# Kernel optimization log

Hardware: AMD Instinct MI355X
Metric: run time of the kernel (lower is better)

## Reference

```python
import jax, jax.numpy as jnp
import numpy as np

N_LVL = [131072, 32768, 8192, 2048, 512, 256]  # active voxels per pyramid level
B = 8          # point clouds in batch
K = 27         # 3x3x3 kernel offsets
SLOPE = 0.01   # LeakyReLU default negative slope
EPS = 1e-5     # BatchNorm eps


def _bn(x, g, b):
    # MinkowskiBatchNorm, training-mode forward: stats over all points
    m = x.mean(0)
    v = x.var(0)
    return (x - m) * jax.lax.rsqrt(v + EPS) * g + b


def _lrelu(x):
    return jnp.where(x >= 0, x, SLOPE * x)


def _lin_block(x, w, g, b):
    # MinkowskiLinear(bias=False) + BN + LeakyReLU (also models 1x1 conv)
    return _lrelu(_bn(x @ w, g, b))


def _conv_block(x, nbr, w, g, b):
    # sparse conv as gather-GEMM: [N,K,Cin] x [K,Cin,Cout] -> [N,Cout]
    y = jnp.einsum('nkc,kco->no', x[nbr], w)
    return _lrelu(_bn(y, g, b))


def _maxpool(x, pmap):
    # stride-2 kernel-3 sparse max pool via precomputed pooling map
    return x[pmap].max(axis=1)


def setup_inputs() -> dict:
    key = jax.random.key(0)
    ks = iter(jax.random.split(key, 80))

    def nrm(shape, scale):
        return jax.random.normal(next(ks), shape, dtype=jnp.float32) * jnp.float32(scale)

    inp = {}
    inp['x'] = nrm((N_LVL[0], 3), 1.0)
    inp['w_mlp1'] = nrm((3, 16), 1.0 / np.sqrt(3.0))
    inp['g_mlp1'] = jnp.ones(16, jnp.float32)
    inp['b_mlp1'] = jnp.zeros(16, jnp.float32)
    conv_dims = [(16, 32), (32, 48), (48, 96), (96, 128), (128, 256), (256, 512)]
    down_dims = [(48, 32), (80, 48), (144, 96), (224, 128), (384, 256)]
    for i, (ci, co) in enumerate(conv_dims):
        inp[f'w_c{i+1}'] = nrm((K, ci, co), np.sqrt(2.0 / (K * co)))  # kaiming fan_out
        inp[f'g_c{i+1}'] = jnp.ones(co, jnp.float32)
        inp[f'b_c{i+1}'] = jnp.zeros(co, jnp.float32)
    for i, (ci, co) in enumerate(down_dims):
        inp[f'w_d{i+1}'] = nrm((ci, co), np.sqrt(2.0 / co))
        inp[f'g_d{i+1}'] = jnp.ones(co, jnp.float32)
        inp[f'b_d{i+1}'] = jnp.zeros(co, jnp.float32)
    inp['w_f1'] = nrm((1024, 512), 1.0 / 32.0)
    inp['g_f1'] = jnp.ones(512, jnp.float32)
    inp['b_f1'] = jnp.zeros(512, jnp.float32)
    inp['w_f2'] = nrm((512, 256), 1.0 / np.sqrt(512.0))
    inp['g_f2'] = jnp.ones(256, jnp.float32)
    inp['b_f2'] = jnp.zeros(256, jnp.float32)
    inp['w_f3'] = nrm((256, 20), 1.0 / 16.0)
    inp['bias_f3'] = jnp.zeros(20, jnp.float32)
    for i in range(6):
        inp[f'nbr{i}'] = jax.random.randint(next(ks), (N_LVL[i], K), 0, N_LVL[i], dtype=jnp.int32)
    for i in range(1, 6):
        inp[f'pool{i}'] = jax.random.randint(next(ks), (N_LVL[i], K), 0, N_LVL[i - 1], dtype=jnp.int32)
    inp['batch5'] = jnp.repeat(jnp.arange(B, dtype=jnp.int32), N_LVL[5] // B)
    return inp


def reference(x, w_mlp1, g_mlp1, b_mlp1,
              w_c1, g_c1, b_c1, w_c2, g_c2, b_c2, w_c3, g_c3, b_c3,
              w_c4, g_c4, b_c4, w_c5, g_c5, b_c5, w_c6, g_c6, b_c6,
              w_d1, g_d1, b_d1, w_d2, g_d2, b_d2, w_d3, g_d3, b_d3,
              w_d4, g_d4, b_d4, w_d5, g_d5, b_d5,
              w_f1, g_f1, b_f1, w_f2, g_f2, b_f2, w_f3, bias_f3,
              nbr0, nbr1, nbr2, nbr3, nbr4, nbr5,
              pool1, pool2, pool3, pool4, pool5, batch5):
    convs = [(w_c1, g_c1, b_c1), (w_c2, g_c2, b_c2), (w_c3, g_c3, b_c3),
             (w_c4, g_c4, b_c4), (w_c5, g_c5, b_c5)]
    downs = [(w_d1, g_d1, b_d1), (w_d2, g_d2, b_d2), (w_d3, g_d3, b_d3),
             (w_d4, g_d4, b_d4), (w_d5, g_d5, b_d5)]
    nbrs = [nbr0, nbr1, nbr2, nbr3, nbr4]
    pools = [pool1, pool2, pool3, pool4, pool5]

    y = _lin_block(x, w_mlp1, g_mlp1, b_mlp1)  # mlp1, level 0
    for i in range(5):  # fixed 5 conv/cat/down/pool stages (structural loop)
        out = _conv_block(y, nbrs[i], *convs[i])
        y = _lin_block(jnp.concatenate([y, out], axis=1), *downs[i])  # cat + down (1x1)
        y = _maxpool(y, pools[i])
    y = _conv_block(y, nbr5, w_c6, g_c6, b_c6)  # conv6 at level 5: [N5, 512]

    xmax = jax.ops.segment_max(y, batch5, num_segments=B)
    cnt = jax.ops.segment_sum(jnp.ones((y.shape[0], 1), y.dtype), batch5, num_segments=B)
    xavg = jax.ops.segment_sum(y, batch5, num_segments=B) / cnt
    z = jnp.concatenate([xmax, xavg], axis=1)  # [B, 1024]

    z = _lin_block(z, w_f1, g_f1, b_f1)  # dropout = identity (eval)
    z = _lin_block(z, w_f2, g_f2, b_f2)
    return z @ w_f3 + bias_f3  # [B, 20] logits
```

## Files before the change

kernel.cpp:

```cpp
#include <hip/hip_runtime.h>
#include <math.h>


#define SLOPE 0.01f
#define BN_EPS 1e-5f

__device__ __forceinline__ void fma4(float s, const float4& w, float4& a) {
    a.x = fmaf(s, w.x, a.x);
    a.y = fmaf(s, w.y, a.y);
    a.z = fmaf(s, w.z, a.z);
    a.w = fmaf(s, w.w, a.w);
}

__global__ void zero_kernel(float* __restrict__ p, int n) {
    int i = blockIdx.x * blockDim.x + threadIdx.x;
    if (i < n) p[i] = 0.f;
}

__global__ void lin_kernel(const float* __restrict__ in, const float* __restrict__ w,
                           float* __restrict__ out, int total, int Cin, int Cout) {
    int stride = gridDim.x * blockDim.x;
    for (int i = blockIdx.x * blockDim.x + threadIdx.x; i < total; i += stride) {
        int n = i / Cout;
        int co = i - n * Cout;
        const float* row = in + n * Cin;
        float acc = 0.f;
        for (int ci = 0; ci < Cin; ci++)
            acc = fmaf(row[ci], w[ci * Cout + co], acc);
        out[i] = acc;
    }
}

__global__ void stats_kernel(const float* __restrict__ x, int total, int C,
                             float* __restrict__ sums) {
    __shared__ float ls[1024];
    int tid = threadIdx.x;
    for (int i = tid; i < 2 * C; i += blockDim.x) ls[i] = 0.f;
    __syncthreads();
    int stride = gridDim.x * blockDim.x;
    int i = blockIdx.x * blockDim.x + tid;
    int c = i % C;
    float s = 0.f, q = 0.f;
    for (; i < total; i += stride) {
        float v = x[i];
        s += v;
        q = fmaf(v, v, q);
    }
    atomicAdd(&ls[c], s);
    atomicAdd(&ls[C + c], q);
    __syncthreads();
    for (int j = tid; j < 2 * C; j += blockDim.x)
        atomicAdd(&sums[j], ls[j]);
}

__global__ void bn_apply_kernel(float* __restrict__ x, int total, int C,
                                const float* __restrict__ sums,
                                const float* __restrict__ g, const float* __restrict__ b,
                                float inv_n) {
    int stride = gridDim.x * blockDim.x;
    for (int i = blockIdx.x * blockDim.x + threadIdx.x; i < total; i += stride) {
        int c = i % C;
        float mean = sums[c] * inv_n;
        float var = fmaf(-mean, mean, sums[C + c] * inv_n);
        var = fmaxf(var, 0.f);
        float scale = g[c] * rsqrtf(var + BN_EPS);
        float v = fmaf(x[i] - mean, scale, b[c]);
        x[i] = v >= 0.f ? v : SLOPE * v;
    }
}

__global__ void maxpool_kernel(const float* __restrict__ in, const int* __restrict__ pmap,
                               float* __restrict__ out, int total, int C) {
    int stride = gridDim.x * blockDim.x;
    for (int i = blockIdx.x * blockDim.x + threadIdx.x; i < total; i += stride) {
        int n = i / C;
        int c = i - n * C;
        const int* pm = pmap + n * 27;
        float m = -INFINITY;
        #pragma unroll
        for (int k = 0; k < 27; k++)
            m = fmaxf(m, in[pm[k] * C + c]);
        out[i] = m;
    }
}

template <int C1, int C2, int COUT>
__global__ void down2_kernel(const float* __restrict__ in1, const float* __restrict__ in2,
                             const float* __restrict__ w, float* __restrict__ out, int Nrows) {
    constexpr int CQT = COUT / 4;
    int i = blockIdx.x * blockDim.x + threadIdx.x;
    if (i >= Nrows * CQT) return;
    int n = i / CQT;
    int coq = i - n * CQT;
    const float4* w4 = reinterpret_cast<const float4*>(w);
    float4 acc = make_float4(0.f, 0.f, 0.f, 0.f);
    const float4* r1 = reinterpret_cast<const float4*>(in1 + n * C1);
    #pragma unroll
    for (int j = 0; j < C1 / 4; j++) {
        float4 a = r1[j];
        fma4(a.x, w4[(4 * j + 0) * CQT + coq], acc);
        fma4(a.y, w4[(4 * j + 1) * CQT + coq], acc);
        fma4(a.z, w4[(4 * j + 2) * CQT + coq], acc);
        fma4(a.w, w4[(4 * j + 3) * CQT + coq], acc);
    }
    const float4* r2 = reinterpret_cast<const float4*>(in2 + n * C2);
    #pragma unroll
    for (int j = 0; j < C2 / 4; j++) {
        float4 a = r2[j];
        int ci = C1 + 4 * j;
        fma4(a.x, w4[(ci + 0) * CQT + coq], acc);
        fma4(a.y, w4[(ci + 1) * CQT + coq], acc);
        fma4(a.z, w4[(ci + 2) * CQT + coq], acc);
        fma4(a.w, w4[(ci + 3) * CQT + coq], acc);
    }
    reinterpret_cast<float4*>(out)[i] = acc;
}

template <int CIN, int COUT, int TM, int CO_TILE, int KT, int NTHR, bool ATOMIC>
__global__ __launch_bounds__(NTHR) void conv2_kernel(
    const float* __restrict__ y, const int* __restrict__ nbr,
    const float* __restrict__ w, float* __restrict__ out) {
    constexpr int CQ = CO_TILE / 4;
    constexpr int MGRP = NTHR / CQ;
    constexpr int RT = TM / MGRP;
    constexpr int LROW = CIN + 4;
    __shared__ __align__(16) float a[TM * LROW];

    const int m0 = blockIdx.x * TM;
    const int cobase = blockIdx.y * CO_TILE;
    const int k0 = blockIdx.z * KT;
    const int tid = threadIdx.x;
    const int coq = tid % CQ;
    const int mg = tid / CQ;

    float4 acc[RT];
    #pragma unroll
    for (int r = 0; r < RT; r++) acc[r] = make_float4(0.f, 0.f, 0.f, 0.f);

    for (int k = k0; k < k0 + KT; k++) {
        __syncthreads();
        for (int idx = tid; idx < TM * (CIN / 4); idx += NTHR) {
            int m = idx / (CIN / 4);
            int c4 = idx - m * (CIN / 4);
            int row = nbr[(m0 + m) * 27 + k];
            float4 v = *reinterpret_cast<const float4*>(y + row * CIN + c4 * 4);
            *reinterpret_cast<float4*>(&a[m * LROW + c4 * 4]) = v;
        }
        __syncthreads();
        const float* wk = w + k * CIN * COUT + cobase + coq * 4;
        #pragma unroll
        for (int ci = 0; ci < CIN; ci += 4) {
            float4 w0 = *reinterpret_cast<const float4*>(wk + (ci + 0) * COUT);
            float4 w1 = *reinterpret_cast<const float4*>(wk + (ci + 1) * COUT);
            float4 w2 = *reinterpret_cast<const float4*>(wk + (ci + 2) * COUT);
            float4 w3 = *reinterpret_cast<const float4*>(wk + (ci + 3) * COUT);
            #pragma unroll
            for (int r = 0; r < RT; r++) {
                const float4 av = *reinterpret_cast<const float4*>(
                    &a[(mg + r * MGRP) * LROW + ci]);
                fma4(av.x, w0, acc[r]);
                fma4(av.y, w1, acc[r]);
                fma4(av.z, w2, acc[r]);
                fma4(av.w, w3, acc[r]);
            }
        }
    }
    #pragma unroll
    for (int r = 0; r < RT; r++) {
        float* op = out + (size_t)(m0 + mg + r * MGRP) * COUT + cobase + coq * 4;
        if (ATOMIC) {
            atomicAdd(op + 0, acc[r].x);
            atomicAdd(op + 1, acc[r].y);
            atomicAdd(op + 2, acc[r].z);
            atomicAdd(op + 3, acc[r].w);
        } else {
            *reinterpret_cast<float4*>(op) = acc[r];
        }
    }
}

__global__ void segpool_kernel(const float* __restrict__ y, float* __restrict__ z) {
    int b = blockIdx.x;
    int c = threadIdx.x;
    float mx = -INFINITY, sm = 0.f;
    for (int r = 0; r < 32; r++) {
        float v = y[(b * 32 + r) * 512 + c];
        mx = fmaxf(mx, v);
        sm += v;
    }
    z[b * 1024 + c] = mx;
    z[b * 1024 + 512 + c] = sm * (1.f / 32.f);
}

template <int K, int COUT, int KSPLIT>
__global__ __launch_bounds__(256) void fc_kernel(const float* __restrict__ z,
                                                 const float* __restrict__ w,
                                                 float* __restrict__ out) {
    constexpr int KC = K / KSPLIT;
    constexpr int KG = KC / 16;
    __shared__ __align__(16) float zt[KC * 8];
    __shared__ float red[16 * 520];

    const int cobase = blockIdx.x * 64;
    const int kc0 = blockIdx.y * KC;
    const int tid = threadIdx.x;
    const int coq = tid & 15;
    const int kg = tid >> 4;

    for (int idx = tid; idx < 8 * (KC / 4); idx += 256) {
        int n = idx / (KC / 4);
        int kq = idx - n * (KC / 4);
        float4 v = *reinterpret_cast<const float4*>(z + n * K + kc0 + kq * 4);
        zt[(kq * 4 + 0) * 8 + n] = v.x;
        zt[(kq * 4 + 1) * 8 + n] = v.y;
        zt[(kq * 4 + 2) * 8 + n] = v.z;
        zt[(kq * 4 + 3) * 8 + n] = v.w;
    }
    __syncthreads();

    float4 acc[8];
    #pragma unroll
    for (int n = 0; n < 8; n++) acc[n] = make_float4(0.f, 0.f, 0.f, 0.f);
    for (int ki = 0; ki < KG; ki++) {
        int k = kg * KG + ki;
        float4 wv = *reinterpret_cast<const float4*>(
            w + (size_t)(kc0 + k) * COUT + cobase + coq * 4);
        float4 za = *reinterpret_cast<const float4*>(&zt[k * 8]);
        float4 zb = *reinterpret_cast<const float4*>(&zt[k * 8 + 4]);
        fma4(za.x, wv, acc[0]);
        fma4(za.y, wv, acc[1]);
        fma4(za.z, wv, acc[2]);
        fma4(za.w, wv, acc[3]);
        fma4(zb.x, wv, acc[4]);
        fma4(zb.y, wv, acc[5]);
        fma4(zb.z, wv, acc[6]);
        fma4(zb.w, wv, acc[7]);
    }
    #pragma unroll
    for (int n = 0; n < 8; n++) {
        red[kg * 520 + (coq * 4 + 0) * 8 + n] = acc[n].x;
        red[kg * 520 + (coq * 4 + 1) * 8 + n] = acc[n].y;
        red[kg * 520 + (coq * 4 + 2) * 8 + n] = acc[n].z;
        red[kg * 520 + (coq * 4 + 3) * 8 + n] = acc[n].w;
    }
    __syncthreads();
    for (int oi = tid; oi < 512; oi += 256) {
        int c = oi >> 3;
        int n = oi & 7;
        float s = 0.f;
        #pragma unroll
        for (int g = 0; g < 16; g++) s += red[g * 520 + c * 8 + n];
        float* op = out + n * COUT + cobase + c;
        if (KSPLIT > 1) atomicAdd(op, s);
        else *op = s;
    }
}

__global__ void f3_kernel(const float* __restrict__ in, const float* __restrict__ w,
                          const float* __restrict__ bias, float* __restrict__ out) {
    int i = blockIdx.x * blockDim.x + threadIdx.x;
    if (i >= 160) return;
    int n = i / 20;
    int co = i - n * 20;
    float acc = bias[co];
    for (int ci = 0; ci < 256; ci++)
        acc = fmaf(in[n * 256 + ci], w[ci * 20 + co], acc);
    out[i] = acc;
}


static inline int stats_block(int C) {
    if (C == 48 || C == 96) return 192;
    if (C == 512) return 512;
    return 256;
}
static inline int capgrid(int total, int block) {
    int g = (total + block - 1) / block;
    return g > 4096 ? 4096 : g;
}

extern "C" void kernel_launch(void* const* d_in, const int* in_sizes, int n_in,
                              void* d_out, int out_size, void* d_ws, size_t ws_size,
                              hipStream_t stream) {
    (void)in_sizes; (void)n_in; (void)out_size; (void)ws_size;

    const int N0 = 131072, N1 = 32768, N2 = 8192, N3 = 2048, N4 = 512, N5 = 256;

    const float* x      = (const float*)d_in[0];
    const float* w_mlp1 = (const float*)d_in[1];
    const float* g_mlp1 = (const float*)d_in[2];
    const float* b_mlp1 = (const float*)d_in[3];
    const float* w_c[6]; const float* g_c[6]; const float* b_c[6];
    for (int i = 0; i < 6; i++) {
        w_c[i] = (const float*)d_in[4 + 3 * i];
        g_c[i] = (const float*)d_in[5 + 3 * i];
        b_c[i] = (const float*)d_in[6 + 3 * i];
    }
    const float* w_d[5]; const float* g_d[5]; const float* b_d[5];
    for (int i = 0; i < 5; i++) {
        w_d[i] = (const float*)d_in[22 + 3 * i];
        g_d[i] = (const float*)d_in[23 + 3 * i];
        b_d[i] = (const float*)d_in[24 + 3 * i];
    }
    const float* w_f1 = (const float*)d_in[37];
    const float* g_f1 = (const float*)d_in[38];
    const float* b_f1 = (const float*)d_in[39];
    const float* w_f2 = (const float*)d_in[40];
    const float* g_f2 = (const float*)d_in[41];
    const float* b_f2 = (const float*)d_in[42];
    const float* w_f3 = (const float*)d_in[43];
    const float* bias_f3 = (const float*)d_in[44];
    const int* nbr[6];
    for (int i = 0; i < 6; i++) nbr[i] = (const int*)d_in[45 + i];
    const int* pool[5];
    for (int i = 0; i < 5; i++) pool[i] = (const int*)d_in[51 + i];

    float* ws    = (float*)d_ws;
    float* bufA  = ws;
    float* bufB  = bufA + 2097152;
    float* bufC  = bufB + 4194304;
    float* stats = bufC + 4194304;
    const int NSTAT = 14 * 1024;
    float* out = (float*)d_out;

    auto run_stats = [&](float* buf, int total, int C, int slot) {
        int bs = stats_block(C);
        int gr = capgrid(total, bs);
        if (gr > 256) gr = 256;
        stats_kernel<<<gr, bs, 0, stream>>>(buf, total, C, stats + slot * 1024);
    };
    auto run_apply = [&](float* buf, int total, int C, int slot,
                         const float* g, const float* b, float inv_n) {
        bn_apply_kernel<<<capgrid(total, 256), 256, 0, stream>>>(
            buf, total, C, stats + slot * 1024, g, b, inv_n);
    };

    zero_kernel<<<(NSTAT + 255) / 256, 256, 0, stream>>>(stats, NSTAT);

    lin_kernel<<<capgrid(N0 * 16, 256), 256, 0, stream>>>(x, w_mlp1, bufA, N0 * 16, 3, 16);
    run_stats(bufA, N0 * 16, 16, 0);
    run_apply(bufA, N0 * 16, 16, 0, g_mlp1, b_mlp1, 1.f / N0);

    conv2_kernel<16, 32, 32, 32, 27, 256, false>
        <<<dim3(N0 / 32, 1, 1), 256, 0, stream>>>(bufA, nbr[0], w_c[0], bufB);
    run_stats(bufB, N0 * 32, 32, 1);
    run_apply(bufB, N0 * 32, 32, 1, g_c[0], b_c[0], 1.f / N0);
    down2_kernel<16, 32, 32><<<capgrid(N0 * 8, 256), 256, 0, stream>>>(bufA, bufB, w_d[0], bufC, N0);
    run_stats(bufC, N0 * 32, 32, 2);
    run_apply(bufC, N0 * 32, 32, 2, g_d[0], b_d[0], 1.f / N0);
    maxpool_kernel<<<capgrid(N1 * 32, 256), 256, 0, stream>>>(bufC, pool[0], bufA, N1 * 32, 32);

    conv2_kernel<32, 48, 32, 48, 27, 192, false>
        <<<dim3(N1 / 32, 1, 1), 192, 0, stream>>>(bufA, nbr[1], w_c[1], bufB);
    run_stats(bufB, N1 * 48, 48, 3);
    run_apply(bufB, N1 * 48, 48, 3, g_c[1], b_c[1], 1.f / N1);
    down2_kernel<32, 48, 48><<<capgrid(N1 * 12, 256), 256, 0, stream>>>(bufA, bufB, w_d[1], bufC, N1);
    run_stats(bufC, N1 * 48, 48, 4);
    run_apply(bufC, N1 * 48, 48, 4, g_d[1], b_d[1], 1.f / N1);
    maxpool_kernel<<<capgrid(N2 * 48, 256), 256, 0, stream>>>(bufC, pool[1], bufA, N2 * 48, 48);

    conv2_kernel<48, 96, 16, 48, 27, 192, false>
        <<<dim3(N2 / 16, 2, 1), 192, 0, stream>>>(bufA, nbr[2], w_c[2], bufB);
    run_stats(bufB, N2 * 96, 96, 5);
    run_apply(bufB, N2 * 96, 96, 5, g_c[2], b_c[2], 1.f / N2);
    down2_kernel<48, 96, 96><<<capgrid(N2 * 24, 256), 256, 0, stream>>>(bufA, bufB, w_d[2], bufC, N2);
    run_stats(bufC, N2 * 96, 96, 6);
    run_apply(bufC, N2 * 96, 96, 6, g_d[2], b_d[2], 1.f / N2);
    maxpool_kernel<<<capgrid(N3 * 96, 256), 256, 0, stream>>>(bufC, pool[2], bufA, N3 * 96, 96);

    zero_kernel<<<(N3 * 128 + 255) / 256, 256, 0, stream>>>(bufB, N3 * 128);
    conv2_kernel<96, 128, 16, 64, 9, 256, true>
        <<<dim3(N3 / 16, 2, 3), 256, 0, stream>>>(bufA, nbr[3], w_c[3], bufB);
    run_stats(bufB, N3 * 128, 128, 7);
    run_apply(bufB, N3 * 128, 128, 7, g_c[3], b_c[3], 1.f / N3);
    down2_kernel<96, 128, 128><<<capgrid(N3 * 32, 256), 256, 0, stream>>>(bufA, bufB, w_d[3], bufC, N3);
    run_stats(bufC, N3 * 128, 128, 8);
    run_apply(bufC, N3 * 128, 128, 8, g_d[3], b_d[3], 1.f / N3);
    maxpool_kernel<<<capgrid(N4 * 128, 256), 256, 0, stream>>>(bufC, pool[3], bufA, N4 * 128, 128);

    zero_kernel<<<(N4 * 256 + 255) / 256, 256, 0, stream>>>(bufB, N4 * 256);
    conv2_kernel<128, 256, 8, 64, 9, 128, true>
        <<<dim3(N4 / 8, 4, 3), 128, 0, stream>>>(bufA, nbr[4], w_c[4], bufB);
    run_stats(bufB, N4 * 256, 256, 9);
    run_apply(bufB, N4 * 256, 256, 9, g_c[4], b_c[4], 1.f / N4);
    down2_kernel<128, 256, 256><<<capgrid(N4 * 64, 256), 256, 0, stream>>>(bufA, bufB, w_d[4], bufC, N4);
    run_stats(bufC, N4 * 256, 256, 10);
    run_apply(bufC, N4 * 256, 256, 10, g_d[4], b_d[4], 1.f / N4);
    maxpool_kernel<<<capgrid(N5 * 256, 256), 256, 0, stream>>>(bufC, pool[4], bufA, N5 * 256, 256);

    zero_kernel<<<(N5 * 512 + 255) / 256, 256, 0, stream>>>(bufB, N5 * 512);
    conv2_kernel<256, 512, 8, 64, 9, 128, true>
        <<<dim3(N5 / 8, 8, 3), 128, 0, stream>>>(bufA, nbr[5], w_c[5], bufB);
    run_stats(bufB, N5 * 512, 512, 11);
    run_apply(bufB, N5 * 512, 512, 11, g_c[5], b_c[5], 1.f / N5);

    segpool_kernel<<<8, 512, 0, stream>>>(bufB, bufC);

    zero_kernel<<<(4096 + 255) / 256, 256, 0, stream>>>(bufA, 4096);
    fc_kernel<1024, 512, 4><<<dim3(8, 4), 256, 0, stream>>>(bufC, w_f1, bufA);
    run_stats(bufA, 8 * 512, 512, 12);
    run_apply(bufA, 8 * 512, 512, 12, g_f1, b_f1, 1.f / 8.f);

    zero_kernel<<<(2048 + 255) / 256, 256, 0, stream>>>(bufB, 2048);
    fc_kernel<512, 256, 4><<<dim3(4, 4), 256, 0, stream>>>(bufA, w_f2, bufB);
    run_stats(bufB, 8 * 256, 256, 13);
    run_apply(bufB, 8 * 256, 256, 13, g_f2, b_f2, 1.f / 8.f);

    f3_kernel<<<1, 192, 0, stream>>>(bufB, w_f3, bias_f3, out);
}
```

Baseline: 1.077 ms.

## Fuse BN+LeakyReLU into consumer kernels and double-buffer sparse conv gathers

Removes the separate BN-apply passes: BN scale/shift and LeakyReLU are now applied on the fly inside the next kernel (conv gather, down projection, pooling, segment pool, FC). The conv kernel gains double-buffered shared-memory gathers with prefetched neighbor indices, multiple output quads per thread and retuned tiles and k-splits. Stats use float4 loads, and mlp1, down and pool get dedicated vectorized kernels. This saves full read/write passes over activations and launch overhead, at the cost of more register and shared-memory pressure and recomputing normalization per gathered element.

```diff
diff --git a/kernel.cpp b/kernel.cpp
--- a/kernel.cpp
+++ b/kernel.cpp
@@ -1,9 +1,8 @@
 #include <hip/hip_runtime.h>
 #include <math.h>
 
-
-#define SLOPE 0.01f
 #define BN_EPS 1e-5f
+
 
 __device__ __forceinline__ void fma4(float s, const float4& w, float4& a) {
     a.x = fmaf(s, w.x, a.x);
@@ -12,190 +11,373 @@
     a.w = fmaf(s, w.w, a.w);
 }
 
+__device__ __forceinline__ float nlr(float x, float sc, float sh) {
+    float t = fmaf(x, sc, sh);
+    return fmaxf(t, 0.01f * t);
+}
+
+__device__ __forceinline__ void bn_coef(const float* __restrict__ sums,
+                                        const float* __restrict__ g,
+                                        const float* __restrict__ b,
+                                        int C, int c, float inv_n,
+                                        float& sc, float& sh) {
+    float mean = sums[c] * inv_n;
+    float var = fmaxf(fmaf(-mean, mean, sums[C + c] * inv_n), 0.f);
+    sc = g[c] * rsqrtf(var + BN_EPS);
+    sh = fmaf(-mean, sc, b[c]);
+}
+
 __global__ void zero_kernel(float* __restrict__ p, int n) {
     int i = blockIdx.x * blockDim.x + threadIdx.x;
     if (i < n) p[i] = 0.f;
 }
 
-__global__ void lin_kernel(const float* __restrict__ in, const float* __restrict__ w,
-                           float* __restrict__ out, int total, int Cin, int Cout) {
-    int stride = gridDim.x * blockDim.x;
-    for (int i = blockIdx.x * blockDim.x + threadIdx.x; i < total; i += stride) {
-        int n = i / Cout;
-        int co = i - n * Cout;
-        const float* row = in + n * Cin;
-        float acc = 0.f;
-        for (int ci = 0; ci < Cin; ci++)
-            acc = fmaf(row[ci], w[ci * Cout + co], acc);
-        out[i] = acc;
-    }
-}
-
-__global__ void stats_kernel(const float* __restrict__ x, int total, int C,
-                             float* __restrict__ sums) {
+__global__ void mlp1_kernel(const float* __restrict__ x, const float* __restrict__ w,
+                            float* __restrict__ out, int N) {
+    int n = blockIdx.x * blockDim.x + threadIdx.x;
+    if (n >= N) return;
+    float x0 = x[n * 3], x1 = x[n * 3 + 1], x2 = x[n * 3 + 2];
+    #pragma unroll
+    for (int c4 = 0; c4 < 4; c4++) {
+        float4 w0 = *reinterpret_cast<const float4*>(w + 0 + c4 * 4);
+        float4 w1 = *reinterpret_cast<const float4*>(w + 16 + c4 * 4);
+        float4 w2 = *reinterpret_cast<const float4*>(w + 32 + c4 * 4);
+        float4 o;
+        o.x = fmaf(x0, w0.x, fmaf(x1, w1.x, x2 * w2.x));
+        o.y = fmaf(x0, w0.y, fmaf(x1, w1.y, x2 * w2.y));
+        o.z = fmaf(x0, w0.z, fmaf(x1, w1.z, x2 * w2.z));
+        o.w = fmaf(x0, w0.w, fmaf(x1, w1.w, x2 * w2.w));
+        *reinterpret_cast<float4*>(out + n * 16 + c4 * 4) = o;
+    }
+}
+
+__global__ void stats4_kernel(const float4* __restrict__ x, int total4, int C, int C4,
+                              float* __restrict__ sums) {
     __shared__ float ls[1024];
     int tid = threadIdx.x;
-    for (int i = tid; i < 2 * C; i += blockDim.x) ls[i] = 0.f;
+    for (int j = tid; j < 2 * C; j += blockDim.x) ls[j] = 0.f;
     __syncthreads();
     int stride = gridDim.x * blockDim.x;
     int i = blockIdx.x * blockDim.x + tid;
-    int c = i % C;
-    float s = 0.f, q = 0.f;
-    for (; i < total; i += stride) {
-        float v = x[i];
-        s += v;
-        q = fmaf(v, v, q);
-    }
-    atomicAdd(&ls[c], s);
-    atomicAdd(&ls[C + c], q);
-    __syncthreads();
-    for (int j = tid; j < 2 * C; j += blockDim.x)
-        atomicAdd(&sums[j], ls[j]);
-}
-
-__global__ void bn_apply_kernel(float* __restrict__ x, int total, int C,
-                                const float* __restrict__ sums,
-                                const float* __restrict__ g, const float* __restrict__ b,
-                                float inv_n) {
-    int stride = gridDim.x * blockDim.x;
-    for (int i = blockIdx.x * blockDim.x + threadIdx.x; i < total; i += stride) {
-        int c = i % C;
-        float mean = sums[c] * inv_n;
-        float var = fmaf(-mean, mean, sums[C + c] * inv_n);
-        var = fmaxf(var, 0.f);
-        float scale = g[c] * rsqrtf(var + BN_EPS);
-        float v = fmaf(x[i] - mean, scale, b[c]);
-        x[i] = v >= 0.f ? v : SLOPE * v;
-    }
-}
-
-__global__ void maxpool_kernel(const float* __restrict__ in, const int* __restrict__ pmap,
-                               float* __restrict__ out, int total, int C) {
-    int stride = gridDim.x * blockDim.x;
-    for (int i = blockIdx.x * blockDim.x + threadIdx.x; i < total; i += stride) {
-        int n = i / C;
-        int c = i - n * C;
-        const int* pm = pmap + n * 27;
-        float m = -INFINITY;
-        #pragma unroll
-        for (int k = 0; k < 27; k++)
-            m = fmaxf(m, in[pm[k] * C + c]);
-        out[i] = m;
-    }
-}
-
-template <int C1, int C2, int COUT>
-__global__ void down2_kernel(const float* __restrict__ in1, const float* __restrict__ in2,
-                             const float* __restrict__ w, float* __restrict__ out, int Nrows) {
-    constexpr int CQT = COUT / 4;
-    int i = blockIdx.x * blockDim.x + threadIdx.x;
-    if (i >= Nrows * CQT) return;
-    int n = i / CQT;
-    int coq = i - n * CQT;
-    const float4* w4 = reinterpret_cast<const float4*>(w);
-    float4 acc = make_float4(0.f, 0.f, 0.f, 0.f);
-    const float4* r1 = reinterpret_cast<const float4*>(in1 + n * C1);
-    #pragma unroll
-    for (int j = 0; j < C1 / 4; j++) {
-        float4 a = r1[j];
-        fma4(a.x, w4[(4 * j + 0) * CQT + coq], acc);
-        fma4(a.y, w4[(4 * j + 1) * CQT + coq], acc);
-        fma4(a.z, w4[(4 * j + 2) * CQT + coq], acc);
-        fma4(a.w, w4[(4 * j + 3) * CQT + coq], acc);
-    }
-    const float4* r2 = reinterpret_cast<const float4*>(in2 + n * C2);
-    #pragma unroll
-    for (int j = 0; j < C2 / 4; j++) {
-        float4 a = r2[j];
-        int ci = C1 + 4 * j;
-        fma4(a.x, w4[(ci + 0) * CQT + coq], acc);
-        fma4(a.y, w4[(ci + 1) * CQT + coq], acc);
-        fma4(a.z, w4[(ci + 2) * CQT + coq], acc);
-        fma4(a.w, w4[(ci + 3) * CQT + coq], acc);
-    }
-    reinterpret_cast<float4*>(out)[i] = acc;
-}
-
-template <int CIN, int COUT, int TM, int CO_TILE, int KT, int NTHR, bool ATOMIC>
-__global__ __launch_bounds__(NTHR) void conv2_kernel(
+    int c4 = i % C4;
+    float4 s = make_float4(0.f, 0.f, 0.f, 0.f);
+    float4 q = make_float4(0.f, 0.f, 0.f, 0.f);
+    for (; i < total4; i += stride) {
+        float4 v = x[i];
+        s.x += v.x; s.y += v.y; s.z += v.z; s.w += v.w;
+        q.x = fmaf(v.x, v.x, q.x); q.y = fmaf(v.y, v.y, q.y);
+        q.z = fmaf(v.z, v.z, q.z); q.w = fmaf(v.w, v.w, q.w);
+    }
+    int cb = c4 * 4;
+    atomicAdd(&ls[cb + 0], s.x); atomicAdd(&ls[cb + 1], s.y);
+    atomicAdd(&ls[cb + 2], s.z); atomicAdd(&ls[cb + 3], s.w);
+    atomicAdd(&ls[C + cb + 0], q.x); atomicAdd(&ls[C + cb + 1], q.y);
+    atomicAdd(&ls[C + cb + 2], q.z); atomicAdd(&ls[C + cb + 3], q.w);
+    __syncthreads();
+    for (int j = tid; j < 2 * C; j += blockDim.x) atomicAdd(&sums[j], ls[j]);
+}
+
+template <int CIN, int COUT, int CO_TILE, int TM, int NTHR, int NQ, int KT,
+          bool NORM_IN, bool ATOMIC>
+__global__ __launch_bounds__(NTHR) void conv3_kernel(
     const float* __restrict__ y, const int* __restrict__ nbr,
-    const float* __restrict__ w, float* __restrict__ out) {
-    constexpr int CQ = CO_TILE / 4;
-    constexpr int MGRP = NTHR / CQ;
+    const float* __restrict__ w, float* __restrict__ out,
+    const float* __restrict__ sums, const float* __restrict__ gg,
+    const float* __restrict__ bb, float inv_n) {
+    constexpr int CQT = CO_TILE / (4 * NQ);
+    constexpr int MGRP = NTHR / CQT;
     constexpr int RT = TM / MGRP;
     constexpr int LROW = CIN + 4;
-    __shared__ __align__(16) float a[TM * LROW];
-
+    constexpr int SLOTS = TM * (CIN / 4);
+    constexpr int GPT = (SLOTS + NTHR - 1) / NTHR;
+
+    __shared__ __align__(16) float a[2][TM * LROW];
+    __shared__ __align__(16) float nsc[CIN], nsh[CIN];
+
+    const int tid = threadIdx.x;
     const int m0 = blockIdx.x * TM;
     const int cobase = blockIdx.y * CO_TILE;
     const int k0 = blockIdx.z * KT;
-    const int tid = threadIdx.x;
-    const int coq = tid % CQ;
-    const int mg = tid / CQ;
-
-    float4 acc[RT];
-    #pragma unroll
-    for (int r = 0; r < RT; r++) acc[r] = make_float4(0.f, 0.f, 0.f, 0.f);
-
-    for (int k = k0; k < k0 + KT; k++) {
-        __syncthreads();
-        for (int idx = tid; idx < TM * (CIN / 4); idx += NTHR) {
-            int m = idx / (CIN / 4);
-            int c4 = idx - m * (CIN / 4);
-            int row = nbr[(m0 + m) * 27 + k];
-            float4 v = *reinterpret_cast<const float4*>(y + row * CIN + c4 * 4);
-            *reinterpret_cast<float4*>(&a[m * LROW + c4 * 4]) = v;
-        }
-        __syncthreads();
-        const float* wk = w + k * CIN * COUT + cobase + coq * 4;
-        #pragma unroll
-        for (int ci = 0; ci < CIN; ci += 4) {
-            float4 w0 = *reinterpret_cast<const float4*>(wk + (ci + 0) * COUT);
-            float4 w1 = *reinterpret_cast<const float4*>(wk + (ci + 1) * COUT);
-            float4 w2 = *reinterpret_cast<const float4*>(wk + (ci + 2) * COUT);
-            float4 w3 = *reinterpret_cast<const float4*>(wk + (ci + 3) * COUT);
+    const int cq = tid % CQT;
+    const int mg = tid / CQT;
+
+    if constexpr (NORM_IN) {
+        for (int c = tid; c < CIN; c += NTHR) {
+            float sc, sh;
+            bn_coef(sums, gg, bb, CIN, c, inv_n, sc, sh);
+            nsc[c] = sc;
+            nsh[c] = sh;
+        }
+    }
+
+    int mj[GPT], c4j[GPT];
+    bool vj[GPT];
+    #pragma unroll
+    for (int j = 0; j < GPT; j++) {
+        int idx = tid + j * NTHR;
+        vj[j] = idx < SLOTS;
+        int ii = vj[j] ? idx : 0;
+        mj[j] = ii / (CIN / 4);
+        c4j[j] = ii % (CIN / 4);
+    }
+
+    int nidx[GPT];
+    #pragma unroll
+    for (int j = 0; j < GPT; j++)
+        if (vj[j]) nidx[j] = nbr[(m0 + mj[j]) * 27 + k0];
+    float4 gv[GPT];
+    #pragma unroll
+    for (int j = 0; j < GPT; j++)
+        if (vj[j]) gv[j] = *reinterpret_cast<const float4*>(
+            y + (size_t)nidx[j] * CIN + c4j[j] * 4);
+    if (KT > 1) {
+        #pragma unroll
+        for (int j = 0; j < GPT; j++)
+            if (vj[j]) nidx[j] = nbr[(m0 + mj[j]) * 27 + k0 + 1];
+    }
+    __syncthreads();
+    #pragma unroll
+    for (int j = 0; j < GPT; j++) {
+        if (!vj[j]) continue;
+        float4 v = gv[j];
+        if constexpr (NORM_IN) {
+            float4 sc = *reinterpret_cast<const float4*>(&nsc[c4j[j] * 4]);
+            float4 sh = *reinterpret_cast<const float4*>(&nsh[c4j[j] * 4]);
+            v.x = nlr(v.x, sc.x, sh.x); v.y = nlr(v.y, sc.y, sh.y);
+            v.z = nlr(v.z, sc.z, sh.z); v.w = nlr(v.w, sc.w, sh.w);
+        }
+        *reinterpret_cast<float4*>(&a[0][mj[j] * LROW + c4j[j] * 4]) = v;
+    }
+    __syncthreads();
+
+    float4 acc[RT][NQ];
+    #pragma unroll
+    for (int r = 0; r < RT; r++)
+        #pragma unroll
+        for (int q = 0; q < NQ; q++) acc[r][q] = make_float4(0.f, 0.f, 0.f, 0.f);
+
+    for (int kk = 0; kk < KT; kk++) {
+        const int cur = kk & 1;
+        if (kk + 1 < KT) {
+            #pragma unroll
+            for (int j = 0; j < GPT; j++)
+                if (vj[j]) gv[j] = *reinterpret_cast<const float4*>(
+                    y + (size_t)nidx[j] * CIN + c4j[j] * 4);
+            if (kk + 2 < KT) {
+                #pragma unroll
+                for (int j = 0; j < GPT; j++)
+                    if (vj[j]) nidx[j] = nbr[(m0 + mj[j]) * 27 + k0 + kk + 2];
+            }
+        }
+        const float* wk = w + (size_t)(k0 + kk) * CIN * COUT + cobase + cq * (4 * NQ);
+        const float* ar = &a[cur][mg * LROW];
+        #pragma unroll 8
+        for (int ci4 = 0; ci4 < CIN / 4; ci4++) {
+            float4 wv[4][NQ];
+            #pragma unroll
+            for (int jj = 0; jj < 4; jj++)
+                #pragma unroll
+                for (int q = 0; q < NQ; q++)
+                    wv[jj][q] = *reinterpret_cast<const float4*>(
+                        wk + (size_t)(ci4 * 4 + jj) * COUT + q * 4);
             #pragma unroll
             for (int r = 0; r < RT; r++) {
-                const float4 av = *reinterpret_cast<const float4*>(
-                    &a[(mg + r * MGRP) * LROW + ci]);
-                fma4(av.x, w0, acc[r]);
-                fma4(av.y, w1, acc[r]);
-                fma4(av.z, w2, acc[r]);
-                fma4(av.w, w3, acc[r]);
+                float4 av = *reinterpret_cast<const float4*>(&ar[r * MGRP * LROW + ci4 * 4]);
+                #pragma unroll
+                for (int q = 0; q < NQ; q++) {
+                    fma4(av.x, wv[0][q], acc[r][q]);
+                    fma4(av.y, wv[1][q], acc[r][q]);
+                    fma4(av.z, wv[2][q], acc[r][q]);
+                    fma4(av.w, wv[3][q], acc[r][q]);
+                }
             }
         }
-    }
-    #pragma unroll
-    for (int r = 0; r < RT; r++) {
-        float* op = out + (size_t)(m0 + mg + r * MGRP) * COUT + cobase + coq * 4;
-        if (ATOMIC) {
-            atomicAdd(op + 0, acc[r].x);
-            atomicAdd(op + 1, acc[r].y);
-            atomicAdd(op + 2, acc[r].z);
-            atomicAdd(op + 3, acc[r].w);
-        } else {
-            *reinterpret_cast<float4*>(op) = acc[r];
-        }
-    }
-}
-
-__global__ void segpool_kernel(const float* __restrict__ y, float* __restrict__ z) {
-    int b = blockIdx.x;
+        if (kk + 1 < KT) {
+            #pragma unroll
+            for (int j = 0; j < GPT; j++) {
+                if (!vj[j]) continue;
+                float4 v = gv[j];
+                if constexpr (NORM_IN) {
+                    float4 sc = *reinterpret_cast<const float4*>(&nsc[c4j[j] * 4]);
+                    float4 sh = *reinterpret_cast<const float4*>(&nsh[c4j[j] * 4]);
+                    v.x = nlr(v.x, sc.x, sh.x); v.y = nlr(v.y, sc.y, sh.y);
+                    v.z = nlr(v.z, sc.z, sh.z); v.w = nlr(v.w, sc.w, sh.w);
+                }
+                *reinterpret_cast<float4*>(&a[cur ^ 1][mj[j] * LROW + c4j[j] * 4]) = v;
+            }
+        }
+        __syncthreads();
+    }
+
+    #pragma unroll
+    for (int r = 0; r < RT; r++)
+        #pragma unroll
+        for (int q = 0; q < NQ; q++) {
+            float* op = out + (size_t)(m0 + mg + r * MGRP) * COUT + cobase + (cq * NQ + q) * 4;
+            if constexpr (ATOMIC) {
+                atomicAdd(op + 0, acc[r][q].x);
+                atomicAdd(op + 1, acc[r][q].y);
+                atomicAdd(op + 2, acc[r][q].z);
+                atomicAdd(op + 3, acc[r][q].w);
+            } else {
+                *reinterpret_cast<float4*>(op) = acc[r][q];
+            }
+        }
+}
+
+template <int C1, int C2, int COUT, int NQ, int NTHR, bool NORM1>
+__global__ __launch_bounds__(NTHR) void down3_kernel(
+    const float* __restrict__ in1, const float* __restrict__ in2,
+    const float* __restrict__ w, float* __restrict__ out,
+    const float* __restrict__ s1, const float* __restrict__ g1,
+    const float* __restrict__ b1, float inv1,
+    const float* __restrict__ s2, const float* __restrict__ g2,
+    const float* __restrict__ b2, float inv2) {
+    constexpr int CQT = COUT / (4 * NQ);
+    constexpr int PAIRS = NTHR / CQT;
+    __shared__ __align__(16) float n1c[C1], n1h[C1], n2c[C2], n2h[C2];
+
+    const int tid = threadIdx.x;
+    if constexpr (NORM1) {
+        for (int c = tid; c < C1; c += NTHR) {
+            float sc, sh;
+            bn_coef(s1, g1, b1, C1, c, inv1, sc, sh);
+            n1c[c] = sc; n1h[c] = sh;
+        }
+    }
+    for (int c = tid; c < C2; c += NTHR) {
+        float sc, sh;
+        bn_coef(s2, g2, b2, C2, c, inv2, sc, sh);
+        n2c[c] = sc; n2h[c] = sh;
+    }
+    __syncthreads();
+
+    const int cq = tid % CQT;
+    const int pr = tid / CQT;
+    const int n0 = (blockIdx.x * PAIRS + pr) * 2;
+
+    float4 acc[2][NQ];
+    #pragma unroll
+    for (int r = 0; r < 2; r++)
+        #pragma unroll
+        for (int q = 0; q < NQ; q++) acc[r][q] = make_float4(0.f, 0.f, 0.f, 0.f);
+
+    const float* w1 = w + cq * (4 * NQ);
+    #pragma unroll 8
+    for (int ci4 = 0; ci4 < C1 / 4; ci4++) {
+        float4 a0 = *reinterpret_cast<const float4*>(in1 + (size_t)n0 * C1 + ci4 * 4);
+        float4 a1 = *reinterpret_cast<const float4*>(in1 + (size_t)(n0 + 1) * C1 + ci4 * 4);
+        if constexpr (NORM1) {
+            float4 sc = *reinterpret_cast<const float4*>(&n1c[ci4 * 4]);
+            float4 sh = *reinterpret_cast<const float4*>(&n1h[ci4 * 4]);
+            a0.x = nlr(a0.x, sc.x, sh.x); a0.y = nlr(a0.y, sc.y, sh.y);
+            a0.z = nlr(a0.z, sc.z, sh.z); a0.w = nlr(a0.w, sc.w, sh.w);
+            a1.x = nlr(a1.x, sc.x, sh.x); a1.y = nlr(a1.y, sc.y, sh.y);
+            a1.z = nlr(a1.z, sc.z, sh.z); a1.w = nlr(a1.w, sc.w, sh.w);
+        }
+        #pragma unroll
+        for (int jj = 0; jj < 4; jj++) {
+            const float* wp = w1 + (size_t)(ci4 * 4 + jj) * COUT;
+            #pragma unroll
+            for (int q = 0; q < NQ; q++) {
+                float4 wv = *reinterpret_cast<const float4*>(wp + q * 4);
+                float e0 = jj == 0 ? a0.x : jj == 1 ? a0.y : jj == 2 ? a0.z : a0.w;
+                float e1 = jj == 0 ? a1.x : jj == 1 ? a1.y : jj == 2 ? a1.z : a1.w;
+                fma4(e0, wv, acc[0][q]);
+                fma4(e1, wv, acc[1][q]);
+            }
+        }
+    }
+    const float* w2 = w + (size_t)C1 * COUT + cq * (4 * NQ);
+    #pragma unroll 8
+    for (int ci4 = 0; ci4 < C2 / 4; ci4++) {
+        float4 a0 = *reinterpret_cast<const float4*>(in2 + (size_t)n0 * C2 + ci4 * 4);
+        float4 a1 = *reinterpret_cast<const float4*>(in2 + (size_t)(n0 + 1) * C2 + ci4 * 4);
+        float4 sc = *reinterpret_cast<const float4*>(&n2c[ci4 * 4]);
+        float4 sh = *reinterpret_cast<const float4*>(&n2h[ci4 * 4]);
+        a0.x = nlr(a0.x, sc.x, sh.x); a0.y = nlr(a0.y, sc.y, sh.y);
+        a0.z = nlr(a0.z, sc.z, sh.z); a0.w = nlr(a0.w, sc.w, sh.w);
+        a1.x = nlr(a1.x, sc.x, sh.x); a1.y = nlr(a1.y, sc.y, sh.y);
+        a1.z = nlr(a1.z, sc.z, sh.z); a1.w = nlr(a1.w, sc.w, sh.w);
+        #pragma unroll
+        for (int jj = 0; jj < 4; jj++) {
+            const float* wp = w2 + (size_t)(ci4 * 4 + jj) * COUT;
+            #pragma unroll
+            for (int q = 0; q < NQ; q++) {
+                float4 wv = *reinterpret_cast<const float4*>(wp + q * 4);
+                float e0 = jj == 0 ? a0.x : jj == 1 ? a0.y : jj == 2 ? a0.z : a0.w;
+                float e1 = jj == 0 ? a1.x : jj == 1 ? a1.y : jj == 2 ? a1.z : a1.w;
+                fma4(e0, wv, acc[0][q]);
+                fma4(e1, wv, acc[1][q]);
+            }
+        }
+    }
+    #pragma unroll
+    for (int r = 0; r < 2; r++)
+        #pragma unroll
+        for (int q = 0; q < NQ; q++)
+            *reinterpret_cast<float4*>(out + (size_t)(n0 + r) * COUT + cq * (4 * NQ) + q * 4) =
+                acc[r][q];
+}
+
+template <int C, int NTHR>
+__global__ __launch_bounds__(NTHR) void pool2_kernel(
+    const float* __restrict__ draw, const int* __restrict__ pmap,
+    const float* __restrict__ sums, const float* __restrict__ g,
+    const float* __restrict__ b, float inv_n,
+    float* __restrict__ yout, int Nout) {
+    constexpr int C4 = C / 4;
+    int i = blockIdx.x * NTHR + threadIdx.x;
+    if (i >= Nout * C4) return;
+    int n = i / C4, c4 = i % C4;
+    float sc[4], sh[4];
+    #pragma unroll
+    for (int j = 0; j < 4; j++) bn_coef(sums, g, b, C, c4 * 4 + j, inv_n, sc[j], sh[j]);
+    const int* pm = pmap + n * 27;
+    float4 mn = make_float4(INFINITY, INFINITY, INFINITY, INFINITY);
+    float4 mx = make_float4(-INFINITY, -INFINITY, -INFINITY, -INFINITY);
+    #pragma unroll 9
+    for (int k = 0; k < 27; k++) {
+        int row = pm[k];
+        float4 v = *reinterpret_cast<const float4*>(draw + (size_t)row * C + c4 * 4);
+        mn.x = fminf(mn.x, v.x); mn.y = fminf(mn.y, v.y);
+        mn.z = fminf(mn.z, v.z); mn.w = fminf(mn.w, v.w);
+        mx.x = fmaxf(mx.x, v.x); mx.y = fmaxf(mx.y, v.y);
+        mx.z = fmaxf(mx.z, v.z); mx.w = fmaxf(mx.w, v.w);
+    }
+    float4 o;
+    o.x = nlr(sc[0] >= 0.f ? mx.x : mn.x, sc[0], sh[0]);
+    o.y = nlr(sc[1] >= 0.f ? mx.y : mn.y, sc[1], sh[1]);
+    o.z = nlr(sc[2] >= 0.f ? mx.z : mn.z, sc[2], sh[2]);
+    o.w = nlr(sc[3] >= 0.f ? mx.w : mn.w, sc[3], sh[3]);
+    *reinterpret_cast<float4*>(yout + (size_t)n * C + c4 * 4) = o;
+}
+
+__global__ void segpool2_kernel(const float* __restrict__ y,
+                                const float* __restrict__ sums,
+                                const float* __restrict__ g, const float* __restrict__ b,
+                                float inv_n, float* __restrict__ z) {
+    int bi = blockIdx.x;
     int c = threadIdx.x;
-    float mx = -INFINITY, sm = 0.f;
+    float sc, sh;
+    bn_coef(sums, g, b, 512, c, inv_n, sc, sh);
+    float mn = INFINITY, mx = -INFINITY, sm = 0.f;
     for (int r = 0; r < 32; r++) {
-        float v = y[(b * 32 + r) * 512 + c];
+        float v = y[(size_t)(bi * 32 + r) * 512 + c];
+        mn = fminf(mn, v);
         mx = fmaxf(mx, v);
-        sm += v;
-    }
-    z[b * 1024 + c] = mx;
-    z[b * 1024 + 512 + c] = sm * (1.f / 32.f);
-}
-
-template <int K, int COUT, int KSPLIT>
-__global__ __launch_bounds__(256) void fc_kernel(const float* __restrict__ z,
-                                                 const float* __restrict__ w,
-                                                 float* __restrict__ out) {
+        sm += nlr(v, sc, sh);
+    }
+    z[bi * 1024 + c] = nlr(sc >= 0.f ? mx : mn, sc, sh);
+    z[bi * 1024 + 512 + c] = sm * (1.f / 32.f);
+}
+
+template <int K, int COUT, int KSPLIT, bool NORM>
+__global__ __launch_bounds__(256) void fc_kernel(
+    const float* __restrict__ z, const float* __restrict__ w,
+    const float* __restrict__ ns, const float* __restrict__ ng,
+    const float* __restrict__ nb, float inv_n,
+    float* __restrict__ out) {
     constexpr int KC = K / KSPLIT;
     constexpr int KG = KC / 16;
     __shared__ __align__(16) float zt[KC * 8];
@@ -210,7 +392,16 @@
     for (int idx = tid; idx < 8 * (KC / 4); idx += 256) {
         int n = idx / (KC / 4);
         int kq = idx - n * (KC / 4);
-        float4 v = *reinterpret_cast<const float4*>(z + n * K + kc0 + kq * 4);
+        float4 v = *reinterpret_cast<const float4*>(z + (size_t)n * K + kc0 + kq * 4);
+        if constexpr (NORM) {
+            #pragma unroll
+            for (int j = 0; j < 4; j++) {
+                float sc, sh;
+                bn_coef(ns, ng, nb, K, kc0 + kq * 4 + j, inv_n, sc, sh);
+                float* pv = j == 0 ? &v.x : j == 1 ? &v.y : j == 2 ? &v.z : &v.w;
+                *pv = nlr(*pv, sc, sh);
+            }
+        }
         zt[(kq * 4 + 0) * 8 + n] = v.x;
         zt[(kq * 4 + 1) * 8 + n] = v.y;
         zt[(kq * 4 + 2) * 8 + n] = v.z;
@@ -227,14 +418,10 @@
             w + (size_t)(kc0 + k) * COUT + cobase + coq * 4);
         float4 za = *reinterpret_cast<const float4*>(&zt[k * 8]);
         float4 zb = *reinterpret_cast<const float4*>(&zt[k * 8 + 4]);
-        fma4(za.x, wv, acc[0]);
-        fma4(za.y, wv, acc[1]);
-        fma4(za.z, wv, acc[2]);
-        fma4(za.w, wv, acc[3]);
-        fma4(zb.x, wv, acc[4]);
-        fma4(zb.y, wv, acc[5]);
-        fma4(zb.z, wv, acc[6]);
-        fma4(zb.w, wv, acc[7]);
+        fma4(za.x, wv, acc[0]); fma4(za.y, wv, acc[1]);
+        fma4(za.z, wv, acc[2]); fma4(za.w, wv, acc[3]);
+        fma4(zb.x, wv, acc[4]); fma4(zb.y, wv, acc[5]);
+        fma4(zb.z, wv, acc[6]); fma4(zb.w, wv, acc[7]);
     }
     #pragma unroll
     for (int n = 0; n < 8; n++) {
@@ -249,35 +436,35 @@
         int n = oi & 7;
         float s = 0.f;
         #pragma unroll
-        for (int g = 0; g < 16; g++) s += red[g * 520 + c * 8 + n];
-        float* op = out + n * COUT + cobase + c;
+        for (int gg = 0; gg < 16; gg++) s += red[gg * 520 + c * 8 + n];
+        float* op = out + (size_t)n * COUT + cobase + c;
         if (KSPLIT > 1) atomicAdd(op, s);
         else *op = s;
     }
 }
 
-__global__ void f3_kernel(const float* __restrict__ in, const float* __restrict__ w,
-                          const float* __restrict__ bias, float* __restrict__ out) {
-    int i = blockIdx.x * blockDim.x + threadIdx.x;
-    if (i >= 160) return;
-    int n = i / 20;
-    int co = i - n * 20;
+__global__ void f3n_kernel(const float* __restrict__ in, const float* __restrict__ w,
+                           const float* __restrict__ bias,
+                           const float* __restrict__ sums, const float* __restrict__ g,
+                           const float* __restrict__ b, float inv_n,
+                           float* __restrict__ out) {
+    __shared__ float zin[8 * 256];
+    int tid = threadIdx.x;
+    for (int idx = tid; idx < 2048; idx += 256) {
+        int c = idx & 255;
+        float sc, sh;
+        bn_coef(sums, g, b, 256, c, inv_n, sc, sh);
+        zin[idx] = nlr(in[idx], sc, sh);
+    }
+    __syncthreads();
+    if (tid >= 160) return;
+    int n = tid / 20, co = tid % 20;
     float acc = bias[co];
     for (int ci = 0; ci < 256; ci++)
-        acc = fmaf(in[n * 256 + ci], w[ci * 20 + co], acc);
-    out[i] = acc;
-}
-
-
-static inline int stats_block(int C) {
-    if (C == 48 || C == 96) return 192;
-    if (C == 512) return 512;
-    return 256;
-}
-static inline int capgrid(int total, int block) {
-    int g = (total + block - 1) / block;
-    return g > 4096 ? 4096 : g;
-}
+        acc = fmaf(zin[n * 256 + ci], w[ci * 20 + co], acc);
+    out[tid] = acc;
+}
+
 
 extern "C" void kernel_launch(void* const* d_in, const int* in_sizes, int n_in,
                               void* d_out, int out_size, void* d_ws, size_t ws_size,
@@ -320,91 +507,98 @@
     float* bufB  = bufA + 2097152;
     float* bufC  = bufB + 4194304;
     float* stats = bufC + 4194304;
-    const int NSTAT = 14 * 1024;
     float* out = (float*)d_out;
 
-    auto run_stats = [&](float* buf, int total, int C, int slot) {
-        int bs = stats_block(C);
-        int gr = capgrid(total, bs);
-        if (gr > 256) gr = 256;
-        stats_kernel<<<gr, bs, 0, stream>>>(buf, total, C, stats + slot * 1024);
+    auto st = [&](int slot) { return stats + slot * 1024; };
+    auto run_stats = [&](const float* buf, int total, int C, int bs, int slot) {
+        int total4 = total / 4, C4 = C / 4;
+        int gr = (total4 + bs - 1) / bs;
+        if (gr > 768) gr = 768;
+        stats4_kernel<<<gr, bs, 0, stream>>>((const float4*)buf, total4, C, C4, st(slot));
     };
-    auto run_apply = [&](float* buf, int total, int C, int slot,
-                         const float* g, const float* b, float inv_n) {
-        bn_apply_kernel<<<capgrid(total, 256), 256, 0, stream>>>(
-            buf, total, C, stats + slot * 1024, g, b, inv_n);
-    };
-
-    zero_kernel<<<(NSTAT + 255) / 256, 256, 0, stream>>>(stats, NSTAT);
-
-    lin_kernel<<<capgrid(N0 * 16, 256), 256, 0, stream>>>(x, w_mlp1, bufA, N0 * 16, 3, 16);
-    run_stats(bufA, N0 * 16, 16, 0);
-    run_apply(bufA, N0 * 16, 16, 0, g_mlp1, b_mlp1, 1.f / N0);
-
-    conv2_kernel<16, 32, 32, 32, 27, 256, false>
-        <<<dim3(N0 / 32, 1, 1), 256, 0, stream>>>(bufA, nbr[0], w_c[0], bufB);
-    run_stats(bufB, N0 * 32, 32, 1);
-    run_apply(bufB, N0 * 32, 32, 1, g_c[0], b_c[0], 1.f / N0);
-    down2_kernel<16, 32, 32><<<capgrid(N0 * 8, 256), 256, 0, stream>>>(bufA, bufB, w_d[0], bufC, N0);
-    run_stats(bufC, N0 * 32, 32, 2);
-    run_apply(bufC, N0 * 32, 32, 2, g_d[0], b_d[0], 1.f / N0);
-    maxpool_kernel<<<capgrid(N1 * 32, 256), 256, 0, stream>>>(bufC, pool[0], bufA, N1 * 32, 32);
-
-    conv2_kernel<32, 48, 32, 48, 27, 192, false>
-        <<<dim3(N1 / 32, 1, 1), 192, 0, stream>>>(bufA, nbr[1], w_c[1], bufB);
-    run_stats(bufB, N1 * 48, 48, 3);
-    run_apply(bufB, N1 * 48, 48, 3, g_c[1], b_c[1], 1.f / N1);
-    down2_kernel<32, 48, 48><<<capgrid(N1 * 12, 256), 256, 0, stream>>>(bufA, bufB, w_d[1], bufC, N1);
-    run_stats(bufC, N1 * 48, 48, 4);
-    run_apply(bufC, N1 * 48, 48, 4, g_d[1], b_d[1], 1.f / N1);
-    maxpool_kernel<<<capgrid(N2 * 48, 256), 256, 0, stream>>>(bufC, pool[1], bufA, N2 * 48, 48);
-
-    conv2_kernel<48, 96, 16, 48, 27, 192, false>
-        <<<dim3(N2 / 16, 2, 1), 192, 0, stream>>>(bufA, nbr[2], w_c[2], bufB);
-    run_stats(bufB, N2 * 96, 96, 5);
-    run_apply(bufB, N2 * 96, 96, 5, g_c[2], b_c[2], 1.f / N2);
-    down2_kernel<48, 96, 96><<<capgrid(N2 * 24, 256), 256, 0, stream>>>(bufA, bufB, w_d[2], bufC, N2);
-    run_stats(bufC, N2 * 96, 96, 6);
-    run_apply(bufC, N2 * 96, 96, 6, g_d[2], b_d[2], 1.f / N2);
-    maxpool_kernel<<<capgrid(N3 * 96, 256), 256, 0, stream>>>(bufC, pool[2], bufA, N3 * 96, 96);
-
-    zero_kernel<<<(N3 * 128 + 255) / 256, 256, 0, stream>>>(bufB, N3 * 128);
-    conv2_kernel<96, 128, 16, 64, 9, 256, true>
-        <<<dim3(N3 / 16, 2, 3), 256, 0, stream>>>(bufA, nbr[3], w_c[3], bufB);
-    run_stats(bufB, N3 * 128, 128, 7);
-    run_apply(bufB, N3 * 128, 128, 7, g_c[3], b_c[3], 1.f / N3);
-    down2_kernel<96, 128, 128><<<capgrid(N3 * 32, 256), 256, 0, stream>>>(bufA, bufB, w_d[3], bufC, N3);
-    run_stats(bufC, N3 * 128, 128, 8);
-    run_apply(bufC, N3 * 128, 128, 8, g_d[3], b_d[3], 1.f / N3);
-    maxpool_kernel<<<capgrid(N4 * 128, 256), 256, 0, stream>>>(bufC, pool[3], bufA, N4 * 128, 128);
-
-    zero_kernel<<<(N4 * 256 + 255) / 256, 256, 0, stream>>>(bufB, N4 * 256);
-    conv2_kernel<128, 256, 8, 64, 9, 128, true>
-        <<<dim3(N4 / 8, 4, 3), 128, 0, stream>>>(bufA, nbr[4], w_c[4], bufB);
-    run_stats(bufB, N4 * 256, 256, 9);
-    run_apply(bufB, N4 * 256, 256, 9, g_c[4], b_c[4], 1.f / N4);
-    down2_kernel<128, 256, 256><<<capgrid(N4 * 64, 256), 256, 0, stream>>>(bufA, bufB, w_d[4], bufC, N4);
-    run_stats(bufC, N4 * 256, 256, 10);
-    run_apply(bufC, N4 * 256, 256, 10, g_d[4], b_d[4], 1.f / N4);
-    maxpool_kernel<<<capgrid(N5 * 256, 256), 256, 0, stream>>>(bufC, pool[4], bufA, N5 * 256, 256);
-
-    zero_kernel<<<(N5 * 512 + 255) / 256, 256, 0, stream>>>(bufB, N5 * 512);
-    conv2_kernel<256, 512, 8, 64, 9, 128, true>
-        <<<dim3(N5 / 8, 8, 3), 128, 0, stream>>>(bufA, nbr[5], w_c[5], bufB);
-    run_stats(bufB, N5 * 512, 512, 11);
-    run_apply(bufB, N5 * 512, 512, 11, g_c[5], b_c[5], 1.f / N5);
-
-    segpool_kernel<<<8, 512, 0, stream>>>(bufB, bufC);
-
-    zero_kernel<<<(4096 + 255) / 256, 256, 0, stream>>>(bufA, 4096);
-    fc_kernel<1024, 512, 4><<<dim3(8, 4), 256, 0, stream>>>(bufC, w_f1, bufA);
-    run_stats(bufA, 8 * 512, 512, 12);
-    run_apply(bufA, 8 * 512, 512, 12, g_f1, b_f1, 1.f / 8.f);
-
-    zero_kernel<<<(2048 + 255) / 256, 256, 0, stream>>>(bufB, 2048);
-    fc_kernel<512, 256, 4><<<dim3(4, 4), 256, 0, stream>>>(bufA, w_f2, bufB);
-    run_stats(bufB, 8 * 256, 256, 13);
-    run_apply(bufB, 8 * 256, 256, 13, g_f2, b_f2, 1.f / 8.f);
-
-    f3_kernel<<<1, 192, 0, stream>>>(bufB, w_f3, bias_f3, out);
-}
+
+    const float iN0 = 1.f / N0, iN1 = 1.f / N1, iN2 = 1.f / N2, iN3 = 1.f / N3,
+                iN4 = 1.f / N4, iN5 = 1.f / N5, i8 = 1.f / 8.f;
+
+    zero_kernel<<<56, 256, 0, stream>>>(stats, 14 * 1024);
+
+    mlp1_kernel<<<N0 / 256, 256, 0, stream>>>(x, w_mlp1, bufA, N0);
+    run_stats(bufA, N0 * 16, 16, 256, 0);
+
+    conv3_kernel<16, 32, 32, 128, 256, 2, 27, true, false>
+        <<<dim3(N0 / 128, 1, 1), 256, 0, stream>>>(bufA, nbr[0], w_c[0], bufB,
+                                                   st(0), g_mlp1, b_mlp1, iN0);
+    run_stats(bufB, N0 * 32, 32, 256, 1);
+    down3_kernel<16, 32, 32, 2, 256, true>
+        <<<1024, 256, 0, stream>>>(bufA, bufB, w_d[0], bufC,
+                                   st(0), g_mlp1, b_mlp1, iN0, st(1), g_c[0], b_c[0], iN0);
+    run_stats(bufC, N0 * 32, 32, 256, 2);
+    pool2_kernel<32, 256><<<N1 * 8 / 256, 256, 0, stream>>>(
+        bufC, pool[0], st(2), g_d[0], b_d[0], iN0, bufA, N1);
+
+    conv3_kernel<32, 48, 48, 64, 192, 2, 27, false, false>
+        <<<dim3(N1 / 64, 1, 1), 192, 0, stream>>>(bufA, nbr[1], w_c[1], bufB,
+                                                  nullptr, nullptr, nullptr, 0.f);
+    run_stats(bufB, N1 * 48, 48, 192, 3);
+    down3_kernel<32, 48, 48, 2, 192, false>
+        <<<512, 192, 0, stream>>>(bufA, bufB, w_d[1], bufC,
+                                  nullptr, nullptr, nullptr, 0.f, st(3), g_c[1], b_c[1], iN1);
+    run_stats(bufC, N1 * 48, 48, 192, 4);
+    pool2_kernel<48, 192><<<N2 * 12 / 192, 192, 0, stream>>>(
+        bufC, pool[1], st(4), g_d[1], b_d[1], iN1, bufA, N2);
+
+    conv3_kernel<48, 96, 48, 64, 192, 2, 27, false, false>
+        <<<dim3(N2 / 64, 2, 1), 192, 0, stream>>>(bufA, nbr[2], w_c[2], bufB,
+                                                  nullptr, nullptr, nullptr, 0.f);
+    run_stats(bufB, N2 * 96, 96, 192, 5);
+    down3_kernel<48, 96, 96, 2, 192, false>
+        <<<256, 192, 0, stream>>>(bufA, bufB, w_d[2], bufC,
+                                  nullptr, nullptr, nullptr, 0.f, st(5), g_c[2], b_c[2], iN2);
+    run_stats(bufC, N2 * 96, 96, 192, 6);
+    pool2_kernel<96, 192><<<N3 * 24 / 192, 192, 0, stream>>>(
+        bufC, pool[2], st(6), g_d[2], b_d[2], iN2, bufA, N3);
+
+    zero_kernel<<<N3 * 128 / 256, 256, 0, stream>>>(bufB, N3 * 128);
+    conv3_kernel<96, 128, 64, 64, 256, 2, 9, false, true>
+        <<<dim3(N3 / 64, 2, 3), 256, 0, stream>>>(bufA, nbr[3], w_c[3], bufB,
+                                                  nullptr, nullptr, nullptr, 0.f);
+    run_stats(bufB, N3 * 128, 128, 256, 7);
+    down3_kernel<96, 128, 128, 2, 256, false>
+        <<<64, 256, 0, stream>>>(bufA, bufB, w_d[3], bufC,
+                                 nullptr, nullptr, nullptr, 0.f, st(7), g_c[3], b_c[3], iN3);
+    run_stats(bufC, N3 * 128, 128, 256, 8);
+    pool2_kernel<128, 256><<<N4 * 32 / 256, 256, 0, stream>>>(
+        bufC, pool[3], st(8), g_d[3], b_d[3], iN3, bufA, N4);
+
+    zero_kernel<<<N4 * 256 / 256, 256, 0, stream>>>(bufB, N4 * 256);
+    conv3_kernel<128, 256, 64, 32, 128, 2, 3, false, true>
+        <<<dim3(N4 / 32, 4, 9), 128, 0, stream>>>(bufA, nbr[4], w_c[4], bufB,
+                                                  nullptr, nullptr, nullptr, 0.f);
+    run_stats(bufB, N4 * 256, 256, 256, 9);
+    down3_kernel<128, 256, 256, 2, 256, false>
+        <<<32, 256, 0, stream>>>(bufA, bufB, w_d[4], bufC,
+                                 nullptr, nullptr, nullptr, 0.f, st(9), g_c[4], b_c[4], iN4);
+    run_stats(bufC, N4 * 256, 256, 256, 10);
+    pool2_kernel<256, 256><<<N5 * 64 / 256, 256, 0, stream>>>(
+        bufC, pool[4], st(10), g_d[4], b_d[4], iN4, bufA, N5);
+
+    zero_kernel<<<N5 * 512 / 256, 256, 0, stream>>>(bufB, N5 * 512);
+    conv3_kernel<256, 512, 64, 16, 128, 1, 3, false, true>
+        <<<dim3(N5 / 16, 8, 9), 128, 0, stream>>>(bufA, nbr[5], w_c[5], bufB,
+                                                  nullptr, nullptr, nullptr, 0.f);
+    run_stats(bufB, N5 * 512, 512, 256, 11);
+
+    segpool2_kernel<<<8, 512, 0, stream>>>(bufB, st(11), g_c[5], b_c[5], iN5, bufC);
+
+    zero_kernel<<<16, 256, 0, stream>>>(bufA, 4096);
+    fc_kernel<1024, 512, 4, false><<<dim3(8, 4), 256, 0, stream>>>(
+        bufC, w_f1, nullptr, nullptr, nullptr, 0.f, bufA);
+    run_stats(bufA, 8 * 512, 512, 256, 12);
+
+    zero_kernel<<<8, 256, 0, stream>>>(bufB, 2048);
+    fc_kernel<512, 256, 4, true><<<dim3(4, 4), 256, 0, stream>>>(
+        bufA, w_f2, st(12), g_f1, b_f1, i8, bufB);
+    run_stats(bufB, 8 * 256, 256, 256, 13);
+
+    f3n_kernel<<<1, 256, 0, stream>>>(bufB, w_f3, bias_f3, st(13), g_f2, b_f2, i8, out);
+}
```

Measured after the change: 1.184 ms. 1.1x slower.
